# Optimization experiments

Hardware: AMD Instinct MI355X
Metric: run time of the kernel (lower is better)

Reference implementation:

```python
import jax, jax.numpy as jnp
import numpy as np

N_NODES = 50000
N_EDGES = 800000
NEG_SLOPE = 0.2


def _gat_layer(x, src, dst, W, a_src, a_dst, bias, heads, out_ch):
    """PyG-style GATConv with self-loops already appended to src/dst."""
    N = x.shape[0]
    h = (x @ W.T).reshape(N, heads, out_ch)            # [N,H,C]
    alpha_src = jnp.einsum('nhc,hc->nh', h, a_src)      # [N,H]
    alpha_dst = jnp.einsum('nhc,hc->nh', h, a_dst)      # [N,H]
    e = jax.nn.leaky_relu(alpha_src[src] + alpha_dst[dst], NEG_SLOPE)  # [E,H]
    # segment softmax over incoming edges of each destination node
    m = jax.ops.segment_max(e, dst, num_segments=N)     # [N,H]
    ex = jnp.exp(e - m[dst])
    denom = jax.ops.segment_sum(ex, dst, num_segments=N)  # [N,H] (>0: self-loops)
    alpha = ex / (denom[dst] + 1e-16)                    # [E,H]
    out = jax.ops.segment_sum(h[src] * alpha[:, :, None], dst, num_segments=N)  # [N,H,C]
    return out.reshape(N, heads * out_ch) + bias


def _with_self_loops(edge_index, n):
    loop = jnp.arange(n, dtype=edge_index.dtype)
    src = jnp.concatenate([edge_index[0], loop])
    dst = jnp.concatenate([edge_index[1], loop])
    return src, dst


def setup_inputs() -> dict:
    key = jax.random.key(0)
    ks = jax.random.split(key, 12)
    s = lambda fan: 1.0 / np.sqrt(fan)
    return {
        'x': jax.random.normal(ks[0], (N_NODES, 16), jnp.float32),
        'edge_index': jax.random.randint(ks[1], (2, N_EDGES), 0, N_NODES, jnp.int64),
        'W1': jax.random.normal(ks[2], (256, 16), jnp.float32) * s(16),
        'att_src1': jax.random.normal(ks[3], (4, 64), jnp.float32) * s(64),
        'att_dst1': jax.random.normal(ks[4], (4, 64), jnp.float32) * s(64),
        'b1': jnp.zeros((256,), jnp.float32),
        'W2': jax.random.normal(ks[5], (64, 256), jnp.float32) * s(256),
        'att_src2': jax.random.normal(ks[6], (1, 64), jnp.float32) * s(64),
        'att_dst2': jax.random.normal(ks[7], (1, 64), jnp.float32) * s(64),
        'b2': jnp.zeros((64,), jnp.float32),
        'fc_w': jax.random.normal(ks[8], (1, 64), jnp.float32) * s(64),
        'fc_b': jnp.zeros((1,), jnp.float32),
    }


def reference(x, edge_index, W1, att_src1, att_dst1, b1,
              W2, att_src2, att_dst2, b2, fc_w, fc_b):
    src, dst = _with_self_loops(edge_index, x.shape[0])
    h = jax.nn.elu(_gat_layer(x, src, dst, W1, att_src1, att_dst1, b1, heads=4, out_ch=64))
    h = jax.nn.elu(_gat_layer(h, src, dst, W2, att_src2, att_dst2, b2, heads=1, out_ch=64))
    return h @ fc_w.T + fc_b
```

## Files before the change

kernel.cpp:

```cpp
#include <hip/hip_runtime.h>
#include <hip/hip_bf16.h>
#include <stdint.h>

#define N_NODES 50000
#define N_EDGES 800000
#define MAXDEG  96
#define NSLICE  6250
#define NSB     196

#define OFF_X    0
#define OFF_W1   800000
#define OFF_AS1  804096
#define OFF_AD1  804352
#define OFF_B1   804608
#define OFF_W2   804864
#define OFF_AS2  821248
#define OFF_AD2  821312
#define OFF_B2   821376
#define OFF_FCW  821440
#define OFF_FCB  821504
#define N_CANON  821505
#define N_W2B    16384
#define N_W1B    16384
#define N_CONV   (N_CANON + N_W2B + N_W1B + N_NODES)

#define TSTRIDE 264

typedef __hip_bfloat16 bf16;
typedef __attribute__((ext_vector_type(8))) short short8;
typedef __attribute__((ext_vector_type(4))) float f32x4;

__device__ __forceinline__ float b2f(bf16 v){ return (float)v; }
__device__ __forceinline__ int clampi(int v, int lo, int hi){ return v < lo ? lo : (v > hi ? hi : v); }
__device__ __forceinline__ float clampf(float v){ return fminf(fmaxf(v, -40.f), 40.f); }
__device__ __forceinline__ uint16_t f2bfbits(float f){
  union { float f; uint32_t u; } c; c.f = f;
  uint32_t r = c.u + 0x7fff + ((c.u >> 16) & 1);
  return (uint16_t)(r >> 16);
}
__device__ __forceinline__ float bitsf(uint32_t u){
  union { uint32_t u; float f; } c; c.u = u; return c.f;
}
__device__ __forceinline__ uint32_t fbits(float f){
  union { float f; uint32_t u; } c; c.f = f; return c.u;
}

__device__ __forceinline__ int load_src(const int* ei, int i, int f){
  return f ? ei[2*(size_t)i] : ei[i];
}
__device__ __forceinline__ int load_dst(const int* ei, int i, int f){
  return f ? ei[2*((size_t)N_EDGES + i)] : ei[N_EDGES + i];
}

__global__ void k_detect(const int* __restrict__ ei, const uint16_t* __restrict__ xu,
                         int* __restrict__ flag){
  const int l = threadIdx.x;
  int or_odd = ei[2*l + 1] | ei[2*(400000 + l) + 1];
  int hits = 0;
  for(int k = 0; k < 64; k++){
    int e = (xu[l*64 + k] >> 7) & 0xFF;
    hits += (e >= 200);
  }
  #pragma unroll
  for(int off=32; off; off>>=1){
    or_odd |= __shfl_xor(or_odd, off, 64);
    hits   += __shfl_xor(hits,   off, 64);
  }
  if(l == 0){
    flag[0] = (or_odd == 0) ? 1 : 0;
    flag[1] = (hits > 16) ? 1 : 0;
  }
}

__global__ void k_convert(const void* x, const void* W1, const void* as1w, const void* ad1w,
                          const void* b1, const void* W2, const void* as2w, const void* ad2w,
                          const void* b2, const void* fcw, const void* fcb,
                          float* __restrict__ canon, uint16_t* __restrict__ W2b,
                          uint16_t* __restrict__ W1b, int* __restrict__ cnt,
                          int* __restrict__ csr_pad, const int* __restrict__ flag){
  int i = blockIdx.x*256 + threadIdx.x;
  int fp32 = flag[1];
  if(i >= N_CANON + N_W2B + N_W1B){
    int j = i - (N_CANON + N_W2B + N_W1B);
    if(j < N_NODES){ cnt[j] = 1; csr_pad[(size_t)j*MAXDEG] = j; }
    return;
  }
  if(i >= N_CANON + N_W2B){
    int j2 = i - (N_CANON + N_W2B);
    int j = j2 >> 6, kk = j2 & 63;
    uint16_t v = 0;
    if((kk >> 4) == (j >> 6)){
      int e = j*16 + (kk & 15);
      v = fp32 ? f2bfbits(((const float*)W1)[e]) : ((const uint16_t*)W1)[e];
    }
    W1b[j2] = v;
    return;
  }
  if(i >= N_CANON){
    int j = i - N_CANON;
    W2b[j] = fp32 ? f2bfbits(((const float*)W2)[j]) : ((const uint16_t*)W2)[j];
    return;
  }
  const void* src; int off;
  if     (i < OFF_W1 ){ src = x;    off = i; }
  else if(i < OFF_AS1){ src = W1;   off = i - OFF_W1; }
  else if(i < OFF_AD1){ src = as1w; off = i - OFF_AS1; }
  else if(i < OFF_B1 ){ src = ad1w; off = i - OFF_AD1; }
  else if(i < OFF_W2 ){ src = b1;   off = i - OFF_B1; }
  else if(i < OFF_AS2){ src = W2;   off = i - OFF_W2; }
  else if(i < OFF_AD2){ src = as2w; off = i - OFF_AS2; }
  else if(i < OFF_B2 ){ src = ad2w; off = i - OFF_AD2; }
  else if(i < OFF_FCW){ src = b2;   off = i - OFF_B2; }
  else if(i < OFF_FCB){ src = fcw;  off = i - OFF_FCW; }
  else               { src = fcb;  off = 0; }
  float v = fp32 ? ((const float*)src)[off] : b2f(((const bf16*)src)[off]);
  canon[i] = v;
}


__global__ __launch_bounds__(256) void k_prepscat(const float* __restrict__ canon,
                        uint32_t* __restrict__ pack, float* __restrict__ dpack,
                        const int* __restrict__ ei, int* __restrict__ cnt,
                        int* __restrict__ csr_pad, const int* __restrict__ flag){
  const int tid = threadIdx.x;
  if(blockIdx.x >= 196){
    const int bid = blockIdx.x - 196;
    const int grp = bid & 7, sb = bid >> 3;
    const int f = flag[0];
    const int lo = grp*NSLICE, hi = lo + NSLICE;
    const int base = sb*4096;
    #pragma unroll 4
    for(int j = 0; j < 16; j++){
      int i = base + j*256 + tid;
      if(i >= N_EDGES) break;
      int d = clampi(load_dst(ei, i, f), 0, N_NODES-1);
      if(d >= lo && d < hi){
        int s = clampi(load_src(ei, i, f), 0, N_NODES-1);
        int pos = atomicAdd(&cnt[d], 1);
        pos = clampi(pos, 0, MAXDEG-1);
        csr_pad[(size_t)d*MAXDEG + pos] = s;
      }
    }
    return;
  }
  __shared__ float ps[64], pd[64];
  if(tid < 128){
    int e = tid & 63;
    int h = e >> 4, k = e & 15;
    const float* av = canon + (tid < 64 ? OFF_AS1 : OFF_AD1) + h*64;
    const float* Wp = canon + OFF_W1 + (h*64)*16 + k;
    float acc = 0.f;
    #pragma unroll 8
    for(int c = 0; c < 64; c++) acc += av[c] * Wp[c*16];
    (tid < 64 ? ps : pd)[e] = acc;
  }
  __syncthreads();
  int n = blockIdx.x*256 + tid;
  if(n >= N_NODES) return;
  float xr[16];
  const float4* xp = (const float4*)(canon + OFF_X + n*16);
  #pragma unroll
  for(int t=0;t<4;t++){ float4 v = xp[t]; xr[4*t]=v.x; xr[4*t+1]=v.y; xr[4*t+2]=v.z; xr[4*t+3]=v.w; }
  uint32_t w[16];
  #pragma unroll
  for(int t=0;t<8;t++)
    w[t] = (uint32_t)f2bfbits(xr[2*t]) | ((uint32_t)f2bfbits(xr[2*t+1]) << 16);
  float qs[8];
  #pragma unroll
  for(int h=0;h<4;h++){
    float a=0.f, b=0.f;
    #pragma unroll
    for(int k=0;k<16;k++){ a += ps[h*16+k]*xr[k]; b += pd[h*16+k]*xr[k]; }
    a = clampf(a); b = clampf(b);
    w[8+2*h]  = fbits(__expf(a));
    w[9+2*h]  = fbits(__expf(0.2f*a));
    qs[2*h]   = __expf(b);
    qs[2*h+1] = __expf(0.2f*b);
  }
  uint4* dst = (uint4*)(pack + (size_t)n*16);
  dst[0] = make_uint4(w[0],w[1],w[2],w[3]);
  dst[1] = make_uint4(w[4],w[5],w[6],w[7]);
  dst[2] = make_uint4(w[8],w[9],w[10],w[11]);
  dst[3] = make_uint4(w[12],w[13],w[14],w[15]);
  float4* dd = (float4*)(dpack + (size_t)n*8);
  dd[0] = make_float4(qs[0],qs[1],qs[2],qs[3]);
  dd[1] = make_float4(qs[4],qs[5],qs[6],qs[7]);
}


struct Ay { float y0,y1,y2,y3,d0,d1,d2,d3; };

__device__ __forceinline__ void edge_acc(const char* __restrict__ r, int k,
                                         float4 qa, float4 qb, bool valid, Ay& a){
  float xv = bitsf((uint32_t)(*(const uint16_t*)(r + k*2)) << 16);
  float4 pa = *(const float4*)(r + 32);
  float4 pb = *(const float4*)(r + 48);
  float w0 = fmaxf(pa.x*qa.x, pa.y*qa.y);
  float w1 = fmaxf(pa.z*qa.z, pa.w*qa.w);
  float w2 = fmaxf(pb.x*qb.x, pb.y*qb.y);
  float w3 = fmaxf(pb.z*qb.z, pb.w*qb.w);
  if(!valid){ w0 = 0.f; w1 = 0.f; w2 = 0.f; w3 = 0.f; }
  a.y0 += w0*xv; a.d0 += w0;
  a.y1 += w1*xv; a.d1 += w1;
  a.y2 += w2*xv; a.d2 += w2;
  a.y3 += w3*xv; a.d3 += w3;
}

__global__ __launch_bounds__(256) void k_aggy(const int* __restrict__ cnt, const int* __restrict__ csr_pad,
                       const uint32_t* __restrict__ pack, const float* __restrict__ dpack,
                       uint16_t* __restrict__ yb){
  const int wv = threadIdx.x >> 6, lane = threadIdx.x & 63;
  const int g = lane >> 4, k = lane & 15;
  const char* pk = (const char*)pack;

  for(int n = blockIdx.x*4 + wv; n < N_NODES; n += gridDim.x*4){
    const int beg = n*MAXDEG;
    const int deg = cnt[n];
    const int end = beg + (deg < MAXDEG ? deg : MAXDEG);
    const float4 qa = *(const float4*)(dpack + (size_t)n*8);
    const float4 qb = *(const float4*)(dpack + (size_t)n*8 + 4);
    Ay a = {0,0,0,0,0,0,0,0};
    int i0 = beg;
    const int nfull = (end - beg) >> 3;
    if(nfull > 0){
      int iA = csr_pad[i0 + g], iB = csr_pad[i0 + 4 + g];
      for(int b = 1; b < nfull; b++){
        int jA = csr_pad[i0 + 8 + g], jB = csr_pad[i0 + 12 + g];
        edge_acc(pk + (size_t)iA*64, k, qa, qb, true, a);
        edge_acc(pk + (size_t)iB*64, k, qa, qb, true, a);
        iA = jA; iB = jB;
        i0 += 8;
      }
      edge_acc(pk + (size_t)iA*64, k, qa, qb, true, a);
      edge_acc(pk + (size_t)iB*64, k, qa, qb, true, a);
      i0 += 8;
    }
    if(i0 < end){
      int iiA = i0 + g, iiB = i0 + 4 + g;
      bool vA = iiA < end, vB = iiB < end;
      int iA = csr_pad[vA ? iiA : end-1];
      int iB = csr_pad[vB ? iiB : end-1];
      edge_acc(pk + (size_t)iA*64, k, qa, qb, vA, a);
      edge_acc(pk + (size_t)iB*64, k, qa, qb, vB, a);
    }
    a.y0 += __shfl_xor(a.y0,16,64); a.y0 += __shfl_xor(a.y0,32,64);
    a.y1 += __shfl_xor(a.y1,16,64); a.y1 += __shfl_xor(a.y1,32,64);
    a.y2 += __shfl_xor(a.y2,16,64); a.y2 += __shfl_xor(a.y2,32,64);
    a.y3 += __shfl_xor(a.y3,16,64); a.y3 += __shfl_xor(a.y3,32,64);
    a.d0 += __shfl_xor(a.d0,16,64); a.d0 += __shfl_xor(a.d0,32,64);
    a.d1 += __shfl_xor(a.d1,16,64); a.d1 += __shfl_xor(a.d1,32,64);
    a.d2 += __shfl_xor(a.d2,16,64); a.d2 += __shfl_xor(a.d2,32,64);
    a.d3 += __shfl_xor(a.d3,16,64); a.d3 += __shfl_xor(a.d3,32,64);
    float yH = (g==0) ? a.y0 : (g==1) ? a.y1 : (g==2) ? a.y2 : a.y3;
    float dH = (g==0) ? a.d0 : (g==1) ? a.d1 : (g==2) ? a.d2 : a.d3;
    yb[(size_t)n*64 + g*16 + k] = f2bfbits(yH / (dH + 1e-16f));
  }
}


__global__ __launch_bounds__(64, 4) void k_mlp(const uint16_t* __restrict__ yb,
                        const uint16_t* __restrict__ W1b, const uint16_t* __restrict__ W2b,
                        const float* __restrict__ canon,
                        bf16* __restrict__ h2, float2* __restrict__ pq2, float2* __restrict__ dq2){
  __shared__ uint16_t tl[16*TSTRIDE];
  const int lane = threadIdx.x & 63;
  const int quad = lane >> 4, c = lane & 15;
  const int n0 = blockIdx.x * 16;

  float b1v[16];
  #pragma unroll
  for(int cb=0; cb<16; cb++) b1v[cb] = canon[OFF_B1 + cb*16 + c];
  float asj[4], adj[4];
  #pragma unroll
  for(int cb=0; cb<4; cb++){
    asj[cb] = canon[OFF_AS2 + cb*16 + c];
    adj[cb] = canon[OFF_AD2 + cb*16 + c];
  }

  short8 af0 = *(const short8*)(yb + (size_t)(n0 + c)*64 + quad*8);
  short8 af1 = *(const short8*)(yb + (size_t)(n0 + c)*64 + 32 + quad*8);
  #pragma unroll
  for(int cb=0; cb<16; cb++){
    short8 wf = *(const short8*)(W1b + (cb*16 + c)*64 + (cb>>3)*32 + quad*8);
    f32x4 acc = (f32x4){0.f,0.f,0.f,0.f};
    acc = __builtin_amdgcn_mfma_f32_16x16x32_bf16((cb>>3) ? af1 : af0, wf, acc, 0,0,0);
    #pragma unroll
    for(int r=0; r<4; r++){
      float o = acc[r] + b1v[cb];
      o = (o > 0.f) ? o : (__expf(o) - 1.f);
      tl[(quad*4 + r)*TSTRIDE + cb*16 + c] = f2bfbits(o);
    }
  }
  f32x4 acc2[4];
  #pragma unroll
  for(int cb=0; cb<4; cb++) acc2[cb] = (f32x4){0.f,0.f,0.f,0.f};
  #pragma unroll
  for(int ks=0; ks<8; ks++){
    short8 af = *(const short8*)(tl + c*TSTRIDE + ks*32 + quad*8);
    #pragma unroll
    for(int cb=0; cb<4; cb++){
      short8 bfrag = *(const short8*)(W2b + (cb*16 + c)*256 + ks*32 + quad*8);
      acc2[cb] = __builtin_amdgcn_mfma_f32_16x16x32_bf16(af, bfrag, acc2[cb], 0,0,0);
    }
  }
  float vs[4] = {0.f,0.f,0.f,0.f}, vd[4] = {0.f,0.f,0.f,0.f};
  #pragma unroll
  for(int cb=0; cb<4; cb++)
    #pragma unroll
    for(int r=0; r<4; r++){
      float v = acc2[cb][r];
      h2[(size_t)(n0 + quad*4 + r)*64 + cb*16 + c] = __float2bfloat16(v);
      vs[r] += v * asj[cb];
      vd[r] += v * adj[cb];
    }
  #pragma unroll
  for(int r=0; r<4; r++){
    #pragma unroll
    for(int off=1; off<16; off<<=1){
      vs[r] += __shfl_xor(vs[r], off, 64);
      vd[r] += __shfl_xor(vd[r], off, 64);
    }
  }
  if(c == 0){
    #pragma unroll
    for(int r=0; r<4; r++){
      float s = clampf(vs[r]), d = clampf(vd[r]);
      pq2[n0 + quad*4 + r] = make_float2(__expf(s), __expf(0.2f*s));
      dq2[n0 + quad*4 + r] = make_float2(__expf(d), __expf(0.2f*d));
    }
  }
}


__global__ __launch_bounds__(256) void k_agg2(const int* __restrict__ cnt, const int* __restrict__ csr_pad,
                       const bf16* __restrict__ h2, const float2* __restrict__ pq2,
                       const float2* __restrict__ dq2, const float* __restrict__ canon,
                       void* __restrict__ outv, const int* __restrict__ flag){
  const int wv = threadIdx.x >> 6, lane = threadIdx.x & 63;
  const int g = lane >> 4, k = lane & 15;
  const char* h2b = (const char*)h2;
  float4 b2v = ((const float4*)(canon + OFF_B2))[k];
  float4 fcv = ((const float4*)(canon + OFF_FCW))[k];
  const float fcb0 = canon[OFF_FCB];
  const int ofp32 = flag[1];
  for(int n = blockIdx.x*4 + wv; n < N_NODES; n += gridDim.x*4){
    const int beg = n*MAXDEG, end = beg + cnt[n];
    const float2 qn = dq2[n];
    float a0=0.f,a1=0.f,a2=0.f,a3=0.f, den=0.f;
    int i0 = beg;
    const int nfull = (end - beg) >> 3;
    if(nfull > 0){
      int iA = csr_pad[i0 + g], iB = csr_pad[i0 + 4 + g];
      for(int b = 1; b < nfull; b++){
        int nA = csr_pad[i0 + 8 + g], nB = csr_pad[i0 + 12 + g];
        uint2 hA = *(const uint2*)(h2b + (size_t)iA*128 + k*8);
        float2 pA = pq2[iA];
        uint2 hB = *(const uint2*)(h2b + (size_t)iB*128 + k*8);
        float2 pB = pq2[iB];
        float wA = fmaxf(pA.x*qn.x, pA.y*qn.y);
        float wB = fmaxf(pB.x*qn.x, pB.y*qn.y);
        den += wA + wB;
        a0 += wA*bitsf(hA.x << 16) + wB*bitsf(hB.x << 16);
        a1 += wA*bitsf(hA.x & 0xffff0000u) + wB*bitsf(hB.x & 0xffff0000u);
        a2 += wA*bitsf(hA.y << 16) + wB*bitsf(hB.y << 16);
        a3 += wA*bitsf(hA.y & 0xffff0000u) + wB*bitsf(hB.y & 0xffff0000u);
        iA = nA; iB = nB;
        i0 += 8;
      }
      {
        uint2 hA = *(const uint2*)(h2b + (size_t)iA*128 + k*8);
        float2 pA = pq2[iA];
        uint2 hB = *(const uint2*)(h2b + (size_t)iB*128 + k*8);
        float2 pB = pq2[iB];
        float wA = fmaxf(pA.x*qn.x, pA.y*qn.y);
        float wB = fmaxf(pB.x*qn.x, pB.y*qn.y);
        den += wA + wB;
        a0 += wA*bitsf(hA.x << 16) + wB*bitsf(hB.x << 16);
        a1 += wA*bitsf(hA.x & 0xffff0000u) + wB*bitsf(hB.x & 0xffff0000u);
        a2 += wA*bitsf(hA.y << 16) + wB*bitsf(hB.y << 16);
        a3 += wA*bitsf(hA.y & 0xffff0000u) + wB*bitsf(hB.y & 0xffff0000u);
        i0 += 8;
      }
    }
    if(i0 < end){
      int iiA = i0 + g, iiB = i0 + 4 + g;
      bool vA = iiA < end, vB = iiB < end;
      int iA = csr_pad[vA ? iiA : end-1];
      int iB = csr_pad[vB ? iiB : end-1];
      uint2 hA = *(const uint2*)(h2b + (size_t)iA*128 + k*8);
      float2 pA = pq2[iA];
      uint2 hB = *(const uint2*)(h2b + (size_t)iB*128 + k*8);
      float2 pB = pq2[iB];
      float wA = vA ? fmaxf(pA.x*qn.x, pA.y*qn.y) : 0.f;
      float wB = vB ? fmaxf(pB.x*qn.x, pB.y*qn.y) : 0.f;
      den += wA + wB;
      a0 += wA*bitsf(hA.x << 16) + wB*bitsf(hB.x << 16);
      a1 += wA*bitsf(hA.x & 0xffff0000u) + wB*bitsf(hB.x & 0xffff0000u);
      a2 += wA*bitsf(hA.y << 16) + wB*bitsf(hB.y << 16);
      a3 += wA*bitsf(hA.y & 0xffff0000u) + wB*bitsf(hB.y & 0xffff0000u);
    }
    a0 += __shfl_xor(a0,16,64); a0 += __shfl_xor(a0,32,64);
    a1 += __shfl_xor(a1,16,64); a1 += __shfl_xor(a1,32,64);
    a2 += __shfl_xor(a2,16,64); a2 += __shfl_xor(a2,32,64);
    a3 += __shfl_xor(a3,16,64); a3 += __shfl_xor(a3,32,64);
    den += __shfl_xor(den,16,64); den += __shfl_xor(den,32,64);
    float inv = 1.f/(den + 1e-16f);
    float o0 = a0*inv + b2v.x, o1 = a1*inv + b2v.y;
    float o2 = a2*inv + b2v.z, o3 = a3*inv + b2v.w;
    o0 = (o0>0.f)?o0:expm1f(o0); o1 = (o1>0.f)?o1:expm1f(o1);
    o2 = (o2>0.f)?o2:expm1f(o2); o3 = (o3>0.f)?o3:expm1f(o3);
    float v = o0*fcv.x + o1*fcv.y + o2*fcv.z + o3*fcv.w;
    v += __shfl_xor(v,1,64); v += __shfl_xor(v,2,64);
    v += __shfl_xor(v,4,64); v += __shfl_xor(v,8,64);
    if(lane == 0){
      float r = v + fcb0;
      if(ofp32) ((float*)outv)[n] = r;
      else      ((bf16*)outv)[n] = __float2bfloat16(r);
    }
  }
}


extern "C" void kernel_launch(void* const* d_in, const int* in_sizes, int n_in,
                              void* d_out, int out_size, void* d_ws, size_t ws_size,
                              hipStream_t stream){
  (void)in_sizes; (void)n_in; (void)out_size;
  const int* ei = (const int*)d_in[1];

  char* w = (char*)d_ws;
  auto carve = [&](size_t bytes)->char*{ char* p = w; w += (bytes + 255) & ~(size_t)255; return p; };
  int*      cnt     = (int*)     carve((size_t)N_NODES*4);
  int*      flag    = (int*)     carve(256);
  int*      csr_pad = (int*)     carve((size_t)N_NODES*MAXDEG*4);
  float*    canon   = (float*)   carve((size_t)N_CANON*4);
  uint16_t* W2b     = (uint16_t*)carve((size_t)N_W2B*2);
  uint16_t* W1b     = (uint16_t*)carve((size_t)N_W1B*2);
  uint32_t* pack    = (uint32_t*)carve((size_t)N_NODES*64);
  float*    dpack   = (float*)   carve((size_t)N_NODES*32);
  uint16_t* yb      = (uint16_t*)carve((size_t)N_NODES*64*2);
  float2*   pq2     = (float2*)  carve((size_t)N_NODES*8);
  float2*   dq2     = (float2*)  carve((size_t)N_NODES*8);
  bf16*     h2      = (bf16*)    carve((size_t)N_NODES*64*2);
  size_t required = (size_t)(w - (char*)d_ws);
  if(ws_size < required) return;

  hipLaunchKernelGGL(k_detect,   dim3(1), dim3(64), 0, stream, ei, (const uint16_t*)d_in[0], flag);
  hipLaunchKernelGGL(k_convert,  dim3((N_CONV+255)/256), dim3(256), 0, stream,
                     d_in[0], d_in[2], d_in[3], d_in[4], d_in[5], d_in[6], d_in[7], d_in[8],
                     d_in[9], d_in[10], d_in[11], canon, W2b, W1b, cnt, csr_pad, flag);
  hipLaunchKernelGGL(k_prepscat, dim3(196 + 8*NSB), dim3(256), 0, stream,
                     canon, pack, dpack, ei, cnt, csr_pad, flag);
  hipLaunchKernelGGL(k_aggy,     dim3(2048), dim3(256), 0, stream, cnt, csr_pad, pack, dpack, yb);
  hipLaunchKernelGGL(k_mlp,      dim3(N_NODES/16), dim3(64), 0, stream, yb, W1b, W2b, canon, h2, pq2, dq2);
  hipLaunchKernelGGL(k_agg2,     dim3(2048), dim3(256), 0, stream, cnt, csr_pad, h2, pq2, dq2, canon, d_out, flag);
}
```

Baseline: 200.3 us.

## Process two destination nodes per wave in aggregation kernels for more gathers in flight

```diff
diff --git a/kernel.cpp b/kernel.cpp
--- a/kernel.cpp
+++ b/kernel.cpp
@@ -188,6 +188,23 @@
 }
 
 
+struct GS { int i0, end, c1, c2; bool v1, v2; };
+
+__device__ __forceinline__ void gs_load(GS& s, const int* __restrict__ csr, int g){
+  int p1 = s.i0 + g, p2 = s.i0 + 4 + g;
+  s.v1 = p1 < s.end; s.v2 = p2 < s.end;
+  s.c1 = csr[s.v1 ? p1 : s.end-1];
+  s.c2 = csr[s.v2 ? p2 : s.end-1];
+}
+__device__ __forceinline__ void gs_init(GS& s, int beg, int deg, const int* __restrict__ csr, int g){
+  s.i0 = beg; s.end = beg + deg;
+  gs_load(s, csr, g);
+}
+__device__ __forceinline__ void gs_step(GS& s, const int* __restrict__ csr, int g){
+  s.i0 += 8; gs_load(s, csr, g);
+}
+
+
 struct Ay { float y0,y1,y2,y3,d0,d1,d2,d3; };
 
 __device__ __forceinline__ void edge_acc(const char* __restrict__ r, int k,
@@ -206,6 +223,20 @@
   a.y3 += w3*xv; a.d3 += w3;
 }
 
+__device__ __forceinline__ void store_y(Ay& a, int n, int g, int k, uint16_t* __restrict__ yb){
+  a.y0 += __shfl_xor(a.y0,16,64); a.y0 += __shfl_xor(a.y0,32,64);
+  a.y1 += __shfl_xor(a.y1,16,64); a.y1 += __shfl_xor(a.y1,32,64);
+  a.y2 += __shfl_xor(a.y2,16,64); a.y2 += __shfl_xor(a.y2,32,64);
+  a.y3 += __shfl_xor(a.y3,16,64); a.y3 += __shfl_xor(a.y3,32,64);
+  a.d0 += __shfl_xor(a.d0,16,64); a.d0 += __shfl_xor(a.d0,32,64);
+  a.d1 += __shfl_xor(a.d1,16,64); a.d1 += __shfl_xor(a.d1,32,64);
+  a.d2 += __shfl_xor(a.d2,16,64); a.d2 += __shfl_xor(a.d2,32,64);
+  a.d3 += __shfl_xor(a.d3,16,64); a.d3 += __shfl_xor(a.d3,32,64);
+  float yH = (g==0) ? a.y0 : (g==1) ? a.y1 : (g==2) ? a.y2 : a.y3;
+  float dH = (g==0) ? a.d0 : (g==1) ? a.d1 : (g==2) ? a.d2 : a.d3;
+  yb[(size_t)n*64 + g*16 + k] = f2bfbits(yH / (dH + 1e-16f));
+}
+
 __global__ __launch_bounds__(256) void k_aggy(const int* __restrict__ cnt, const int* __restrict__ csr_pad,
                        const uint32_t* __restrict__ pack, const float* __restrict__ dpack,
                        uint16_t* __restrict__ yb){
@@ -213,47 +244,32 @@
   const int g = lane >> 4, k = lane & 15;
   const char* pk = (const char*)pack;
 
-  for(int n = blockIdx.x*4 + wv; n < N_NODES; n += gridDim.x*4){
-    const int beg = n*MAXDEG;
-    const int deg = cnt[n];
-    const int end = beg + (deg < MAXDEG ? deg : MAXDEG);
-    const float4 qa = *(const float4*)(dpack + (size_t)n*8);
-    const float4 qb = *(const float4*)(dpack + (size_t)n*8 + 4);
-    Ay a = {0,0,0,0,0,0,0,0};
-    int i0 = beg;
-    const int nfull = (end - beg) >> 3;
-    if(nfull > 0){
-      int iA = csr_pad[i0 + g], iB = csr_pad[i0 + 4 + g];
-      for(int b = 1; b < nfull; b++){
-        int jA = csr_pad[i0 + 8 + g], jB = csr_pad[i0 + 12 + g];
-        edge_acc(pk + (size_t)iA*64, k, qa, qb, true, a);
-        edge_acc(pk + (size_t)iB*64, k, qa, qb, true, a);
-        iA = jA; iB = jB;
-        i0 += 8;
-      }
-      edge_acc(pk + (size_t)iA*64, k, qa, qb, true, a);
-      edge_acc(pk + (size_t)iB*64, k, qa, qb, true, a);
-      i0 += 8;
-    }
-    if(i0 < end){
-      int iiA = i0 + g, iiB = i0 + 4 + g;
-      bool vA = iiA < end, vB = iiB < end;
-      int iA = csr_pad[vA ? iiA : end-1];
-      int iB = csr_pad[vB ? iiB : end-1];
-      edge_acc(pk + (size_t)iA*64, k, qa, qb, vA, a);
-      edge_acc(pk + (size_t)iB*64, k, qa, qb, vB, a);
-    }
-    a.y0 += __shfl_xor(a.y0,16,64); a.y0 += __shfl_xor(a.y0,32,64);
-    a.y1 += __shfl_xor(a.y1,16,64); a.y1 += __shfl_xor(a.y1,32,64);
-    a.y2 += __shfl_xor(a.y2,16,64); a.y2 += __shfl_xor(a.y2,32,64);
-    a.y3 += __shfl_xor(a.y3,16,64); a.y3 += __shfl_xor(a.y3,32,64);
-    a.d0 += __shfl_xor(a.d0,16,64); a.d0 += __shfl_xor(a.d0,32,64);
-    a.d1 += __shfl_xor(a.d1,16,64); a.d1 += __shfl_xor(a.d1,32,64);
-    a.d2 += __shfl_xor(a.d2,16,64); a.d2 += __shfl_xor(a.d2,32,64);
-    a.d3 += __shfl_xor(a.d3,16,64); a.d3 += __shfl_xor(a.d3,32,64);
-    float yH = (g==0) ? a.y0 : (g==1) ? a.y1 : (g==2) ? a.y2 : a.y3;
-    float dH = (g==0) ? a.d0 : (g==1) ? a.d1 : (g==2) ? a.d2 : a.d3;
-    yb[(size_t)n*64 + g*16 + k] = f2bfbits(yH / (dH + 1e-16f));
+  for(int np = blockIdx.x*4 + wv; np < N_NODES/2; np += gridDim.x*4){
+    const int nA = np*2, nB = nA + 1;
+    int degA = cnt[nA]; degA = degA < MAXDEG ? degA : MAXDEG;
+    int degB = cnt[nB]; degB = degB < MAXDEG ? degB : MAXDEG;
+    const float4 qaA = *(const float4*)(dpack + (size_t)nA*8);
+    const float4 qbA = *(const float4*)(dpack + (size_t)nA*8 + 4);
+    const float4 qaB = *(const float4*)(dpack + (size_t)nB*8);
+    const float4 qbB = *(const float4*)(dpack + (size_t)nB*8 + 4);
+    Ay aA = {0,0,0,0,0,0,0,0}, aB = {0,0,0,0,0,0,0,0};
+    GS A, B;
+    gs_init(A, nA*MAXDEG, degA, csr_pad, g);
+    gs_init(B, nB*MAXDEG, degB, csr_pad, g);
+    const int dmax = degA > degB ? degA : degB;
+    const int nb = (dmax + 7) >> 3;
+    for(int bb = 0; bb < nb; bb++){
+      int ac1 = A.c1, ac2 = A.c2; bool av1 = A.v1, av2 = A.v2;
+      int bc1 = B.c1, bc2 = B.c2; bool bv1 = B.v1, bv2 = B.v2;
+      gs_step(A, csr_pad, g);
+      gs_step(B, csr_pad, g);
+      edge_acc(pk + (size_t)ac1*64, k, qaA, qbA, av1, aA);
+      edge_acc(pk + (size_t)ac2*64, k, qaA, qbA, av2, aA);
+      edge_acc(pk + (size_t)bc1*64, k, qaB, qbB, bv1, aB);
+      edge_acc(pk + (size_t)bc2*64, k, qaB, qbB, bv2, aB);
+    }
+    store_y(aA, nA, g, k, yb);
+    store_y(aB, nB, g, k, yb);
   }
 }
 
@@ -331,6 +347,44 @@
   }
 }
 
+
+__device__ __forceinline__ void edge_acc2(const char* __restrict__ h2b,
+                                          const float2* __restrict__ pq2,
+                                          int i, int k, float2 qn, bool valid,
+                                          float& a0, float& a1, float& a2, float& a3, float& den){
+  uint2 h = *(const uint2*)(h2b + (size_t)i*128 + k*8);
+  float2 p = pq2[i];
+  float w = fmaxf(p.x*qn.x, p.y*qn.y);
+  if(!valid) w = 0.f;
+  den += w;
+  a0 += w*bitsf(h.x << 16);
+  a1 += w*bitsf(h.x & 0xffff0000u);
+  a2 += w*bitsf(h.y << 16);
+  a3 += w*bitsf(h.y & 0xffff0000u);
+}
+
+__device__ __forceinline__ void finish2(float a0, float a1, float a2, float a3, float den,
+                                        float4 b2v, float4 fcv, float fcb0, int lane,
+                                        int n, void* __restrict__ outv, int ofp32){
+  a0 += __shfl_xor(a0,16,64); a0 += __shfl_xor(a0,32,64);
+  a1 += __shfl_xor(a1,16,64); a1 += __shfl_xor(a1,32,64);
+  a2 += __shfl_xor(a2,16,64); a2 += __shfl_xor(a2,32,64);
+  a3 += __shfl_xor(a3,16,64); a3 += __shfl_xor(a3,32,64);
+  den += __shfl_xor(den,16,64); den += __shfl_xor(den,32,64);
+  float inv = 1.f/(den + 1e-16f);
+  float o0 = a0*inv + b2v.x, o1 = a1*inv + b2v.y;
+  float o2 = a2*inv + b2v.z, o3 = a3*inv + b2v.w;
+  o0 = (o0>0.f)?o0:expm1f(o0); o1 = (o1>0.f)?o1:expm1f(o1);
+  o2 = (o2>0.f)?o2:expm1f(o2); o3 = (o3>0.f)?o3:expm1f(o3);
+  float v = o0*fcv.x + o1*fcv.y + o2*fcv.z + o3*fcv.w;
+  v += __shfl_xor(v,1,64); v += __shfl_xor(v,2,64);
+  v += __shfl_xor(v,4,64); v += __shfl_xor(v,8,64);
+  if(lane == 0){
+    float r = v + fcb0;
+    if(ofp32) ((float*)outv)[n] = r;
+    else      ((bf16*)outv)[n] = __float2bfloat16(r);
+  }
+}
 
 __global__ __launch_bounds__(256) void k_agg2(const int* __restrict__ cnt, const int* __restrict__ csr_pad,
                        const bf16* __restrict__ h2, const float2* __restrict__ pq2,
@@ -343,80 +397,31 @@
   float4 fcv = ((const float4*)(canon + OFF_FCW))[k];
   const float fcb0 = canon[OFF_FCB];
   const int ofp32 = flag[1];
-  for(int n = blockIdx.x*4 + wv; n < N_NODES; n += gridDim.x*4){
-    const int beg = n*MAXDEG, end = beg + cnt[n];
-    const float2 qn = dq2[n];
-    float a0=0.f,a1=0.f,a2=0.f,a3=0.f, den=0.f;
-    int i0 = beg;
-    const int nfull = (end - beg) >> 3;
-    if(nfull > 0){
-      int iA = csr_pad[i0 + g], iB = csr_pad[i0 + 4 + g];
-      for(int b = 1; b < nfull; b++){
-        int nA = csr_pad[i0 + 8 + g], nB = csr_pad[i0 + 12 + g];
-        uint2 hA = *(const uint2*)(h2b + (size_t)iA*128 + k*8);
-        float2 pA = pq2[iA];
-        uint2 hB = *(const uint2*)(h2b + (size_t)iB*128 + k*8);
-        float2 pB = pq2[iB];
-        float wA = fmaxf(pA.x*qn.x, pA.y*qn.y);
-        float wB = fmaxf(pB.x*qn.x, pB.y*qn.y);
-        den += wA + wB;
-        a0 += wA*bitsf(hA.x << 16) + wB*bitsf(hB.x << 16);
-        a1 += wA*bitsf(hA.x & 0xffff0000u) + wB*bitsf(hB.x & 0xffff0000u);
-        a2 += wA*bitsf(hA.y << 16) + wB*bitsf(hB.y << 16);
-        a3 += wA*bitsf(hA.y & 0xffff0000u) + wB*bitsf(hB.y & 0xffff0000u);
-        iA = nA; iB = nB;
-        i0 += 8;
-      }
-      {
-        uint2 hA = *(const uint2*)(h2b + (size_t)iA*128 + k*8);
-        float2 pA = pq2[iA];
-        uint2 hB = *(const uint2*)(h2b + (size_t)iB*128 + k*8);
-        float2 pB = pq2[iB];
-        float wA = fmaxf(pA.x*qn.x, pA.y*qn.y);
-        float wB = fmaxf(pB.x*qn.x, pB.y*qn.y);
-        den += wA + wB;
-        a0 += wA*bitsf(hA.x << 16) + wB*bitsf(hB.x << 16);
-        a1 += wA*bitsf(hA.x & 0xffff0000u) + wB*bitsf(hB.x & 0xffff0000u);
-        a2 += wA*bitsf(hA.y << 16) + wB*bitsf(hB.y << 16);
-        a3 += wA*bitsf(hA.y & 0xffff0000u) + wB*bitsf(hB.y & 0xffff0000u);
-        i0 += 8;
-      }
-    }
-    if(i0 < end){
-      int iiA = i0 + g, iiB = i0 + 4 + g;
-      bool vA = iiA < end, vB = iiB < end;
-      int iA = csr_pad[vA ? iiA : end-1];
-      int iB = csr_pad[vB ? iiB : end-1];
-      uint2 hA = *(const uint2*)(h2b + (size_t)iA*128 + k*8);
-      float2 pA = pq2[iA];
-      uint2 hB = *(const uint2*)(h2b + (size_t)iB*128 + k*8);
-      float2 pB = pq2[iB];
-      float wA = vA ? fmaxf(pA.x*qn.x, pA.y*qn.y) : 0.f;
-      float wB = vB ? fmaxf(pB.x*qn.x, pB.y*qn.y) : 0.f;
-      den += wA + wB;
-      a0 += wA*bitsf(hA.x << 16) + wB*bitsf(hB.x << 16);
-      a1 += wA*bitsf(hA.x & 0xffff0000u) + wB*bitsf(hB.x & 0xffff0000u);
-      a2 += wA*bitsf(hA.y << 16) + wB*bitsf(hB.y << 16);
-      a3 += wA*bitsf(hA.y & 0xffff0000u) + wB*bitsf(hB.y & 0xffff0000u);
-    }
-    a0 += __shfl_xor(a0,16,64); a0 += __shfl_xor(a0,32,64);
-    a1 += __shfl_xor(a1,16,64); a1 += __shfl_xor(a1,32,64);
-    a2 += __shfl_xor(a2,16,64); a2 += __shfl_xor(a2,32,64);
-    a3 += __shfl_xor(a3,16,64); a3 += __shfl_xor(a3,32,64);
-    den += __shfl_xor(den,16,64); den += __shfl_xor(den,32,64);
-    float inv = 1.f/(den + 1e-16f);
-    float o0 = a0*inv + b2v.x, o1 = a1*inv + b2v.y;
-    float o2 = a2*inv + b2v.z, o3 = a3*inv + b2v.w;
-    o0 = (o0>0.f)?o0:expm1f(o0); o1 = (o1>0.f)?o1:expm1f(o1);
-    o2 = (o2>0.f)?o2:expm1f(o2); o3 = (o3>0.f)?o3:expm1f(o3);
-    float v = o0*fcv.x + o1*fcv.y + o2*fcv.z + o3*fcv.w;
-    v += __shfl_xor(v,1,64); v += __shfl_xor(v,2,64);
-    v += __shfl_xor(v,4,64); v += __shfl_xor(v,8,64);
-    if(lane == 0){
-      float r = v + fcb0;
-      if(ofp32) ((float*)outv)[n] = r;
-      else      ((bf16*)outv)[n] = __float2bfloat16(r);
-    }
+
+  for(int np = blockIdx.x*4 + wv; np < N_NODES/2; np += gridDim.x*4){
+    const int nA = np*2, nB = nA + 1;
+    int degA = cnt[nA]; degA = degA < MAXDEG ? degA : MAXDEG;
+    int degB = cnt[nB]; degB = degB < MAXDEG ? degB : MAXDEG;
+    const float2 qnA = dq2[nA], qnB = dq2[nB];
+    float aA0=0.f,aA1=0.f,aA2=0.f,aA3=0.f,dA=0.f;
+    float aB0=0.f,aB1=0.f,aB2=0.f,aB3=0.f,dB=0.f;
+    GS A, B;
+    gs_init(A, nA*MAXDEG, degA, csr_pad, g);
+    gs_init(B, nB*MAXDEG, degB, csr_pad, g);
+    const int dmax = degA > degB ? degA : degB;
+    const int nb = (dmax + 7) >> 3;
+    for(int bb = 0; bb < nb; bb++){
+      int ac1 = A.c1, ac2 = A.c2; bool av1 = A.v1, av2 = A.v2;
+      int bc1 = B.c1, bc2 = B.c2; bool bv1 = B.v1, bv2 = B.v2;
+      gs_step(A, csr_pad, g);
+      gs_step(B, csr_pad, g);
+      edge_acc2(h2b, pq2, ac1, k, qnA, av1, aA0, aA1, aA2, aA3, dA);
+      edge_acc2(h2b, pq2, ac2, k, qnA, av2, aA0, aA1, aA2, aA3, dA);
+      edge_acc2(h2b, pq2, bc1, k, qnB, bv1, aB0, aB1, aB2, aB3, dB);
+      edge_acc2(h2b, pq2, bc2, k, qnB, bv2, aB0, aB1, aB2, aB3, dB);
+    }
+    finish2(aA0, aA1, aA2, aA3, dA, b2v, fcv, fcb0, lane, nA, outv, ofp32);
+    finish2(aB0, aB1, aB2, aB3, dB, b2v, fcv, fcb0, lane, nB, outv, ofp32);
   }
 }
 
```

New measurement: 215.2 us. +7.4%, slower.
